# Kernel optimization log

Hardware: AMD Instinct MI355X
Metric: run time of the kernel (lower is better)

Reference implementation:

```python
import jax, jax.numpy as jnp
import numpy as np

N = 100000
IN_C = 128
HID = 32   # 2*out_channels
OUT = 16
NEG_SLOPE = 0.2


def gat_layer(x, src, dst, n, W, a_src, a_dst, b):
    # x: [n, Cin] -> h: [n, Cout]
    h = x @ W
    alpha_s = h @ a_src  # [n]
    alpha_d = h @ a_dst  # [n]
    e = jax.nn.leaky_relu(alpha_s[src] + alpha_d[dst], NEG_SLOPE)  # [E]
    # softmax over edges grouped by destination node (self-loops ensure no empty groups)
    m = jax.ops.segment_max(e, dst, num_segments=n)
    ex = jnp.exp(e - m[dst])
    s = jax.ops.segment_sum(ex, dst, num_segments=n)
    alpha = ex / s[dst]  # [E]
    out = jax.ops.segment_sum(h[src] * alpha[:, None], dst, num_segments=n)
    return out + b


def setup_inputs() -> dict:
    key = jax.random.key(0)
    ks = jax.random.split(key, 16)
    x = jax.random.normal(ks[0], (N, IN_C), dtype=jnp.float32)
    edge_index = jax.random.randint(ks[1], (2, 1600000), 0, N, dtype=jnp.int64)

    def glorot(k, shape):
        fan = shape[0] + (shape[1] if len(shape) > 1 else 1)
        return jax.random.normal(k, shape, dtype=jnp.float32) * jnp.sqrt(2.0 / fan)

    return {
        "x": x,
        "edge_index": edge_index,
        "W1": glorot(ks[2], (IN_C, HID)),
        "a1_src": glorot(ks[3], (HID,)),
        "a1_dst": glorot(ks[4], (HID,)),
        "b1": jnp.zeros((HID,), dtype=jnp.float32),
        "W_mu": glorot(ks[5], (HID, OUT)),
        "a_mu_src": glorot(ks[6], (OUT,)),
        "a_mu_dst": glorot(ks[7], (OUT,)),
        "b_mu": jnp.zeros((OUT,), dtype=jnp.float32),
        "W_ls": glorot(ks[8], (HID, OUT)),
        "a_ls_src": glorot(ks[9], (OUT,)),
        "a_ls_dst": glorot(ks[10], (OUT,)),
        "b_ls": jnp.zeros((OUT,), dtype=jnp.float32),
    }


def reference(x, edge_index, W1, a1_src, a1_dst, b1,
              W_mu, a_mu_src, a_mu_dst, b_mu,
              W_ls, a_ls_src, a_ls_dst, b_ls):
    n = x.shape[0]
    # PyG GATConv default: add self-loops
    loop = jnp.arange(n, dtype=edge_index.dtype)
    src = jnp.concatenate([edge_index[0], loop])
    dst = jnp.concatenate([edge_index[1], loop])

    h = jax.nn.relu(gat_layer(x, src, dst, n, W1, a1_src, a1_dst, b1))
    mu = gat_layer(h, src, dst, n, W_mu, a_mu_src, a_mu_dst, b_mu)
    logstd = gat_layer(h, src, dst, n, W_ls, a_ls_src, a_ls_dst, b_ls)
    return (mu, logstd)
```

## Files before the change

kernel.cpp:

```cpp
#include <hip/hip_runtime.h>
#include <hip/hip_bf16.h>
#include <hip/hip_fp16.h>

typedef unsigned int u32;
typedef unsigned short u16;

__device__ __forceinline__ float lrelu(float v) {
    return v > 0.f ? v : 0.2f * v;
}

__device__ __forceinline__ float4 ldq_h16(const u16* __restrict__ row, int q) {
    uint2 u = ((const uint2*)row)[q];
    __half2 a = *(__half2*)&u.x;
    __half2 b = *(__half2*)&u.y;
    float2 fa = __half22float2(a);
    float2 fb = __half22float2(b);
    return make_float4(fa.x, fa.y, fb.x, fb.y);
}

__device__ __forceinline__ u32 pack2h(float x, float y) {
    __half2 h = __float22half2_rn(make_float2(x, y));
    return *(u32*)&h;
}

#define PCHUNK 4096
#define NW 256

__global__ __launch_bounds__(256) void g1p_kernel(
    const float* __restrict__ x, const float* __restrict__ W,
    const float* __restrict__ a_src, const float* __restrict__ a_dst,
    u16* __restrict__ h16, float* __restrict__ as_, float* __restrict__ ad_,
    const int* __restrict__ srcI, const int* __restrict__ dstI,
    u32* __restrict__ pairs, u32* __restrict__ bcur,
    int n, int E, int wsz, int cap, int pgrid)
{
    __shared__ float xs[64][132];
    __shared__ float Wl[128][32];
    __shared__ float asv[32], adv[32];
    __shared__ u32 lcount[NW];
    __shared__ u32 lbase[NW];
    int t = threadIdx.x;

    if ((int)blockIdx.x < pgrid) {
        int chunk = blockIdx.x * PCHUNK;
        lcount[t] = 0;
        __syncthreads();
        u32 pk[16]; int wv[16]; u32 rk[16]; bool val[16];
#pragma unroll
        for (int k = 0; k < 16; k++) {
            int i = chunk + k * 256 + t;
            val[k] = i < E;
            if (val[k]) {
                u32 s = (u32)srcI[i];
                u32 d = (u32)dstI[i];
                wv[k] = d / (u32)wsz;
                u32 dloc = d - (u32)wv[k] * (u32)wsz;
                pk[k] = (dloc << 17) | s;
                rk[k] = atomicAdd(&lcount[wv[k]], 1u);
            }
        }
        __syncthreads();
        if (lcount[t] > 0)
            lbase[t] = atomicAdd(&bcur[t], lcount[t]);
        __syncthreads();
#pragma unroll
        for (int k = 0; k < 16; k++) {
            if (val[k]) {
                u32 pos = lbase[wv[k]] + rk[k];
                if (pos < (u32)cap)
                    pairs[(size_t)wv[k] * cap + pos] = pk[k];
            }
        }
        return;
    }

    int rb = (blockIdx.x - pgrid) * 64;

    for (int i = t; i < 4096; i += 256) Wl[i >> 5][i & 31] = W[i];
    if (t < 32) { asv[t] = a_src[t]; adv[t] = a_dst[t]; }
    for (int i = t; i < 2048; i += 256) {
        int row = i >> 5, seg = i & 31;
        float4 v = make_float4(0.f, 0.f, 0.f, 0.f);
        if (rb + row < n)
            v = ((const float4*)(x + (size_t)(rb + row) * 128))[seg];
        int c = seg * 4;
        xs[row][c + 0] = v.x; xs[row][c + 1] = v.y;
        xs[row][c + 2] = v.z; xs[row][c + 3] = v.w;
    }
    __syncthreads();

    int tr = t >> 3;
    int tc = t & 7;
    float acc[2][4];
#pragma unroll
    for (int i = 0; i < 2; i++)
#pragma unroll
        for (int j = 0; j < 4; j++) acc[i][j] = 0.f;

#pragma unroll 4
    for (int k = 0; k < 128; k++) {
        float x0 = xs[tr][k];
        float x1 = xs[tr + 32][k];
        float4 wv = *(const float4*)&Wl[k][tc * 4];
        acc[0][0] += x0 * wv.x; acc[0][1] += x0 * wv.y;
        acc[0][2] += x0 * wv.z; acc[0][3] += x0 * wv.w;
        acc[1][0] += x1 * wv.x; acc[1][1] += x1 * wv.y;
        acc[1][2] += x1 * wv.z; acc[1][3] += x1 * wv.w;
    }

#pragma unroll
    for (int i = 0; i < 2; i++) {
        int r = rb + tr + i * 32;
        if (r < n) {
            uint2 p;
            p.x = pack2h(acc[i][0], acc[i][1]);
            p.y = pack2h(acc[i][2], acc[i][3]);
            *(uint2*)&h16[(size_t)r * 32 + tc * 4] = p;
        }
        float ps = 0.f, pd = 0.f;
#pragma unroll
        for (int j = 0; j < 4; j++) {
            int c = tc * 4 + j;
            ps += acc[i][j] * asv[c];
            pd += acc[i][j] * adv[c];
        }
        for (int m = 1; m < 8; m <<= 1) {
            ps += __shfl_xor(ps, m, 64);
            pd += __shfl_xor(pd, m, 64);
        }
        if (tc == 0 && r < n) { as_[r] = ps; ad_[r] = pd; }
    }
}

__global__ __launch_bounds__(256) void csr_window_kernel(
    const u32* __restrict__ pairs, const u32* __restrict__ bcur,
    u32* __restrict__ rowS, u32* __restrict__ deg, int* __restrict__ srcS,
    int n, int wsz, int cap)
{
    __shared__ u32 dw[512];
    __shared__ u32 cw[512];
    __shared__ u32 ts[256];
    int grp = blockIdx.x;
    int t = threadIdx.x;
    int wlo = grp * wsz;
    int wnodes = n - wlo; if (wnodes < 0) wnodes = 0; if (wnodes > wsz) wnodes = wsz;
    u32 cnt = bcur[grp]; if (cnt > (u32)cap) cnt = (u32)cap;
    size_t base = (size_t)grp * cap;

    {
        int wlo_t = t * wsz;
        int wn_t = n - wlo_t; if (wn_t < 0) wn_t = 0; if (wn_t > wsz) wn_t = wsz;
        u32 c_t = bcur[t]; if (c_t > (u32)cap) c_t = (u32)cap;
        ts[t] = c_t + (u32)wn_t;
        __syncthreads();
        for (int o = 1; o < NW; o <<= 1) {
            u32 y = (t >= o) ? ts[t - o] : 0u;
            __syncthreads();
            ts[t] += y;
            __syncthreads();
        }
    }
    u32 wb = ts[grp] - (cnt + (u32)wnodes);
    __syncthreads();

    dw[t] = 0; dw[t + 256] = 0;
    __syncthreads();
    for (u32 i = t; i < cnt; i += 256)
        atomicAdd(&dw[pairs[base + i] >> 17], 1u);
    __syncthreads();

    int i0 = 2 * t, i1 = 2 * t + 1;
    u32 e0 = (i0 < wnodes) ? dw[i0] + 1u : 0u;
    u32 e1 = (i1 < wnodes) ? dw[i1] + 1u : 0u;
    ts[t] = e0 + e1;
    __syncthreads();
    for (int o = 1; o < 256; o <<= 1) {
        u32 y = (t >= o) ? ts[t - o] : 0u;
        __syncthreads();
        ts[t] += y;
        __syncthreads();
    }
    u32 off = wb + ts[t] - (e0 + e1);
    if (i0 < wnodes) {
        u32 dgi = dw[i0];
        cw[i0] = off;
        rowS[wlo + i0] = off;
        deg[wlo + i0] = dgi;
        srcS[off + dgi] = wlo + i0;
    }
    u32 off1 = off + e0;
    if (i1 < wnodes) {
        u32 dgi = dw[i1];
        cw[i1] = off1;
        rowS[wlo + i1] = off1;
        deg[wlo + i1] = dgi;
        srcS[off1 + dgi] = wlo + i1;
    }
    __syncthreads();

    for (u32 i = t; i < cnt; i += 256) {
        u32 pr = pairs[base + i];
        u32 pos = atomicAdd(&cw[pr >> 17], 1u);
        srcS[pos] = (int)(pr & 0x1FFFFu);
    }
}

__global__ __launch_bounds__(256) void l1_fused_kernel(
    const u32* __restrict__ rowS, const u32* __restrict__ deg,
    const int* __restrict__ srcS,
    const float* __restrict__ as_, const float* __restrict__ ad_,
    const u16* __restrict__ h16, const float* __restrict__ b1,
    float* __restrict__ h1r, int n)
{
    int d = blockIdx.x * 16 + (threadIdx.x >> 4);
    if (d >= n) return;
    int l  = threadIdx.x & 15;
    int e2 = l >> 3;
    int q  = l & 7;
    int gb = (threadIdx.x & 63) & 48;

    int beg = (int)rowS[d];
    int end = beg + (int)deg[d] + 1;
    float adv = ad_[d];

    float wsum = 0.f;
    float4 acc = make_float4(0.f, 0.f, 0.f, 0.f);

    for (int tb = beg; tb < end; tb += 16) {
        int j = tb + l;
        bool valid = j < end;
        int s = valid ? srcS[j] : 0;
        float p = valid ? __expf(fminf(lrelu(as_[s] + adv), 60.f)) : 0.f;
        int cnt = end - tb; if (cnt > 16) cnt = 16;
        for (int jj = 0; jj < cnt; jj += 2) {
            int idx = jj + e2;
            int sj  = __shfl(s, gb + idx, 64);
            float w = __shfl(p, gb + idx, 64);
            if (idx >= cnt) w = 0.f;
            wsum += w;
            float4 hv = ldq_h16(h16 + (size_t)sj * 32, q);
            acc.x += w * hv.x; acc.y += w * hv.y;
            acc.z += w * hv.z; acc.w += w * hv.w;
        }
    }
    wsum  += __shfl_xor(wsum, 8, 64);
    acc.x += __shfl_xor(acc.x, 8, 64);
    acc.y += __shfl_xor(acc.y, 8, 64);
    acc.z += __shfl_xor(acc.z, 8, 64);
    acc.w += __shfl_xor(acc.w, 8, 64);
    if (l < 8) {
        float inv = 1.f / wsum;
        float4 r;
        r.x = fmaxf(acc.x * inv + b1[4 * q + 0], 0.f);
        r.y = fmaxf(acc.y * inv + b1[4 * q + 1], 0.f);
        r.z = fmaxf(acc.z * inv + b1[4 * q + 2], 0.f);
        r.w = fmaxf(acc.w * inv + b1[4 * q + 3], 0.f);
        *(float4*)&h1r[(size_t)d * 32 + 4 * q] = r;
    }
}

__global__ __launch_bounds__(256) void gemm2_kernel(
    const float* __restrict__ h1r,
    const float* __restrict__ Wm, const float* __restrict__ Wl_,
    const float* __restrict__ ams, const float* __restrict__ amd,
    const float* __restrict__ alsb, const float* __restrict__ ald,
    u16* __restrict__ hmhl16, float2* __restrict__ attn2,
    float* __restrict__ amud, float* __restrict__ alsd, int n)
{
    __shared__ float hs[16][33];
    __shared__ float Wms[32][16], Wls[32][16];
    __shared__ float amsv[16], amdv[16], alsv[16], aldv[16];
    int t = threadIdx.x;
    int rb = blockIdx.x * 16;

    for (int i = t; i < 512; i += 256) {
        int k = i >> 4, c = i & 15;
        Wms[k][c] = Wm[i];
        Wls[k][c] = Wl_[i];
    }
    if (t < 16) {
        amsv[t] = ams[t]; amdv[t] = amd[t];
        alsv[t] = alsb[t]; aldv[t] = ald[t];
    }
    for (int i = t; i < 512; i += 256) {
        int r = i >> 5, k = i & 31;
        int gr = rb + r;
        hs[r][k] = (gr < n) ? h1r[(size_t)gr * 32 + k] : 0.f;
    }
    __syncthreads();

    int tr = t >> 4;
    int c = t & 15;
    float accm = 0.f, accl = 0.f;
#pragma unroll
    for (int k = 0; k < 32; k++) {
        float hv = hs[tr][k];
        accm += hv * Wms[k][c];
        accl += hv * Wls[k][c];
    }
    int r = rb + tr;
    if (r < n) {
        hmhl16[(size_t)r * 32 + c]      = __half_as_ushort(__float2half(accm));
        hmhl16[(size_t)r * 32 + 16 + c] = __half_as_ushort(__float2half(accl));
    }
    float pms = accm * amsv[c], pmd = accm * amdv[c];
    float pls = accl * alsv[c], pld = accl * aldv[c];
    for (int m = 1; m < 16; m <<= 1) {
        pms += __shfl_xor(pms, m, 64);
        pmd += __shfl_xor(pmd, m, 64);
        pls += __shfl_xor(pls, m, 64);
        pld += __shfl_xor(pld, m, 64);
    }
    if (c == 0 && r < n) {
        attn2[r] = make_float2(pms, pls);
        amud[r] = pmd;
        alsd[r] = pld;
    }
}

__global__ __launch_bounds__(256) void l2_fused_kernel(
    const u32* __restrict__ rowS, const u32* __restrict__ deg,
    const int* __restrict__ srcS,
    const float2* __restrict__ attn2,
    const float* __restrict__ amud, const float* __restrict__ alsd,
    const u16* __restrict__ hmhl16,
    const float* __restrict__ bm, const float* __restrict__ bl,
    float* __restrict__ out, int n)
{
    int d = blockIdx.x * 16 + (threadIdx.x >> 4);
    if (d >= n) return;
    int l  = threadIdx.x & 15;
    int e2 = l >> 3;
    int q  = l & 7;
    int gb = (threadIdx.x & 63) & 48;
    bool isMu = q < 4;

    int beg = (int)rowS[d];
    int end = beg + (int)deg[d] + 1;
    float amdv = amud[d], aldv = alsd[d];

    float wsum = 0.f;
    float4 acc = make_float4(0.f, 0.f, 0.f, 0.f);

    for (int tb = beg; tb < end; tb += 16) {
        int j = tb + l;
        bool valid = j < end;
        int s = valid ? srcS[j] : 0;
        float2 a2 = valid ? attn2[s] : make_float2(0.f, 0.f);
        float pm = valid ? __expf(fminf(lrelu(a2.x + amdv), 60.f)) : 0.f;
        float pl = valid ? __expf(fminf(lrelu(a2.y + aldv), 60.f)) : 0.f;
        int cnt = end - tb; if (cnt > 16) cnt = 16;
        for (int jj = 0; jj < cnt; jj += 2) {
            int idx = jj + e2;
            int sj    = __shfl(s, gb + idx, 64);
            float pmj = __shfl(pm, gb + idx, 64);
            float plj = __shfl(pl, gb + idx, 64);
            float w = isMu ? pmj : plj;
            if (idx >= cnt) w = 0.f;
            wsum += w;
            float4 hv = ldq_h16(hmhl16 + (size_t)sj * 32, q);
            acc.x += w * hv.x; acc.y += w * hv.y;
            acc.z += w * hv.z; acc.w += w * hv.w;
        }
    }
    wsum  += __shfl_xor(wsum, 8, 64);
    acc.x += __shfl_xor(acc.x, 8, 64);
    acc.y += __shfl_xor(acc.y, 8, 64);
    acc.z += __shfl_xor(acc.z, 8, 64);
    acc.w += __shfl_xor(acc.w, 8, 64);
    if (l < 8) {
        float inv = 1.f / wsum;
        if (q < 4) {
            float4 r;
            r.x = acc.x * inv + bm[4 * q + 0];
            r.y = acc.y * inv + bm[4 * q + 1];
            r.z = acc.z * inv + bm[4 * q + 2];
            r.w = acc.w * inv + bm[4 * q + 3];
            *(float4*)&out[(size_t)d * 16 + 4 * q] = r;
        } else {
            int qc = 4 * (q - 4);
            float4 r;
            r.x = acc.x * inv + bl[qc + 0];
            r.y = acc.y * inv + bl[qc + 1];
            r.z = acc.z * inv + bl[qc + 2];
            r.w = acc.w * inv + bl[qc + 3];
            *(float4*)&out[(size_t)n * 16 + (size_t)d * 16 + qc] = r;
        }
    }
}

extern "C" void kernel_launch(void* const* d_in, const int* in_sizes, int n_in,
                              void* d_out, int out_size, void* d_ws, size_t ws_size,
                              hipStream_t stream)
{
    const float* x   = (const float*)d_in[0];
    const int*   ei  = (const int*)d_in[1];
    const float* W1  = (const float*)d_in[2];
    const float* a1s = (const float*)d_in[3];
    const float* a1d = (const float*)d_in[4];
    const float* b1  = (const float*)d_in[5];
    const float* Wm  = (const float*)d_in[6];
    const float* ams = (const float*)d_in[7];
    const float* amd = (const float*)d_in[8];
    const float* bm  = (const float*)d_in[9];
    const float* Wl  = (const float*)d_in[10];
    const float* als = (const float*)d_in[11];
    const float* ald = (const float*)d_in[12];
    const float* bl  = (const float*)d_in[13];

    int n  = in_sizes[0] / 128;
    int E  = in_sizes[1] / 2;
    int Et = E + n;
    int wsz = (n + NW - 1) / NW;
    int cap = E / NW + 3072;
    const int* srcI = ei;
    const int* dstI = ei + E;

    float* ws = (float*)d_ws;
    u16*    h16   = (u16*)ws;
    u16*    hmhl16 = (u16*)(ws + (size_t)16 * n);
    float*  h1r  = ws + (size_t)32 * n;
    u32*    pairs = (u32*)(ws + (size_t)32 * n);
    float*  as_  = ws + (size_t)64 * n;
    float*  ad_  = ws + (size_t)65 * n;
    float2* attn2 = (float2*)(ws + (size_t)64 * n);
    float*  amud = ws + (size_t)66 * n;
    float*  alsd = ws + (size_t)67 * n;
    u32*    deg  = (u32*)(ws + (size_t)68 * n);
    u32*    bcur = (u32*)(ws + (size_t)69 * n);
    u32*    rowS = (u32*)(ws + (size_t)70 * n);
    int*    srcS = (int*)(ws + (size_t)71 * n);

    int pgrid = (E + PCHUNK - 1) / PCHUNK;
    int gblocks = (n + 63) / 64;

    hipMemsetAsync(bcur, 0, NW * sizeof(u32), stream);

    g1p_kernel<<<pgrid + gblocks, 256, 0, stream>>>(
        x, W1, a1s, a1d, h16, as_, ad_,
        srcI, dstI, pairs, bcur, n, E, wsz, cap, pgrid);

    csr_window_kernel<<<NW, 256, 0, stream>>>(pairs, bcur,
                                              rowS, deg, srcS, n, wsz, cap);

    l1_fused_kernel<<<(n + 15) / 16, 256, 0, stream>>>(rowS, deg, srcS, as_, ad_,
                                                       h16, b1, h1r, n);

    gemm2_kernel<<<(n + 15) / 16, 256, 0, stream>>>(h1r, Wm, Wl, ams, amd, als, ald,
                                                    hmhl16, attn2, amud, alsd, n);

    l2_fused_kernel<<<(n + 15) / 16, 256, 0, stream>>>(rowS, deg, srcS,
                                                       attn2, amud, alsd,
                                                       hmhl16, bm, bl,
                                                       (float*)d_out, n);
}
```

Measured before the change: 257.0 us.

## Sort destination nodes by degree within each window for balanced aggregation

The CSR build kernel now runs a per-window counting sort of destination nodes by in-degree and writes a permutation array. Both aggregation kernels read this permutation, so 16-lane groups in the same wavefront handle nodes with similar degree. The goal is less loop divergence and imbalance inside wavefronts. The cost is extra histogram and scan work in the CSR kernel, an extra indirection per node, and scattered writes to the output rows.

```diff
diff --git a/kernel.cpp b/kernel.cpp
--- a/kernel.cpp
+++ b/kernel.cpp
@@ -135,11 +135,13 @@
 __global__ __launch_bounds__(256) void csr_window_kernel(
     const u32* __restrict__ pairs, const u32* __restrict__ bcur,
     u32* __restrict__ rowS, u32* __restrict__ deg, int* __restrict__ srcS,
+    u32* __restrict__ perm,
     int n, int wsz, int cap)
 {
     __shared__ u32 dw[512];
     __shared__ u32 cw[512];
     __shared__ u32 ts[256];
+    __shared__ u32 hb[512];
     int grp = blockIdx.x;
     int t = threadIdx.x;
     int wlo = grp * wsz;
@@ -164,6 +166,7 @@
     __syncthreads();
 
     dw[t] = 0; dw[t + 256] = 0;
+    hb[t] = 0; hb[t + 256] = 0;
     __syncthreads();
     for (u32 i = t; i < cnt; i += 256)
         atomicAdd(&dw[pairs[base + i] >> 17], 1u);
@@ -198,6 +201,33 @@
     }
     __syncthreads();
 
+    for (int i = t; i < wnodes; i += 256)
+        atomicAdd(&hb[dw[i] < 511u ? dw[i] : 511u], 1u);
+    __syncthreads();
+    {
+        u32 h0 = hb[2 * t], h1 = hb[2 * t + 1];
+        ts[t] = h0 + h1;
+        __syncthreads();
+        for (int o = 1; o < 256; o <<= 1) {
+            u32 y = (t >= o) ? ts[t - o] : 0u;
+            __syncthreads();
+            ts[t] += y;
+            __syncthreads();
+        }
+        u32 b0 = ts[t] - (h0 + h1);
+        hb[2 * t] = b0;
+        hb[2 * t + 1] = b0 + h0;
+    }
+    __syncthreads();
+    for (int i = t; i < wnodes; i += 256) {
+        u32 dg = dw[i] < 511u ? dw[i] : 511u;
+        u32 pos = atomicAdd(&hb[dg], 1u);
+        perm[wlo + pos] = (u32)(wlo + i);
+    }
+    for (int i = wnodes + t; i < wsz; i += 256)
+        perm[wlo + i] = 0x7fffffffu;
+    __syncthreads();
+
     for (u32 i = t; i < cnt; i += 256) {
         u32 pr = pairs[base + i];
         u32 pos = atomicAdd(&cw[pr >> 17], 1u);
@@ -207,12 +237,14 @@
 
 __global__ __launch_bounds__(256) void l1_fused_kernel(
     const u32* __restrict__ rowS, const u32* __restrict__ deg,
-    const int* __restrict__ srcS,
+    const int* __restrict__ srcS, const u32* __restrict__ perm,
     const float* __restrict__ as_, const float* __restrict__ ad_,
     const u16* __restrict__ h16, const float* __restrict__ b1,
-    float* __restrict__ h1r, int n)
-{
-    int d = blockIdx.x * 16 + (threadIdx.x >> 4);
+    float* __restrict__ h1r, int n, int ntot)
+{
+    int gid = blockIdx.x * 16 + (threadIdx.x >> 4);
+    if (gid >= ntot) return;
+    int d = (int)perm[gid];
     if (d >= n) return;
     int l  = threadIdx.x & 15;
     int e2 = l >> 3;
@@ -320,14 +352,16 @@
 
 __global__ __launch_bounds__(256) void l2_fused_kernel(
     const u32* __restrict__ rowS, const u32* __restrict__ deg,
-    const int* __restrict__ srcS,
+    const int* __restrict__ srcS, const u32* __restrict__ perm,
     const float2* __restrict__ attn2,
     const float* __restrict__ amud, const float* __restrict__ alsd,
     const u16* __restrict__ hmhl16,
     const float* __restrict__ bm, const float* __restrict__ bl,
-    float* __restrict__ out, int n)
-{
-    int d = blockIdx.x * 16 + (threadIdx.x >> 4);
+    float* __restrict__ out, int n, int ntot)
+{
+    int gid = blockIdx.x * 16 + (threadIdx.x >> 4);
+    if (gid >= ntot) return;
+    int d = (int)perm[gid];
     if (d >= n) return;
     int l  = threadIdx.x & 15;
     int e2 = l >> 3;
@@ -413,6 +447,7 @@
     int Et = E + n;
     int wsz = (n + NW - 1) / NW;
     int cap = E / NW + 3072;
+    int ntot = NW * wsz;
     const int* srcI = ei;
     const int* dstI = ei + E;
 
@@ -430,6 +465,7 @@
     u32*    bcur = (u32*)(ws + (size_t)69 * n);
     u32*    rowS = (u32*)(ws + (size_t)70 * n);
     int*    srcS = (int*)(ws + (size_t)71 * n);
+    u32*    perm = (u32*)(ws + (size_t)71 * n + Et);
 
     int pgrid = (E + PCHUNK - 1) / PCHUNK;
     int gblocks = (n + 63) / 64;
@@ -441,16 +477,18 @@
         srcI, dstI, pairs, bcur, n, E, wsz, cap, pgrid);
 
     csr_window_kernel<<<NW, 256, 0, stream>>>(pairs, bcur,
-                                              rowS, deg, srcS, n, wsz, cap);
-
-    l1_fused_kernel<<<(n + 15) / 16, 256, 0, stream>>>(rowS, deg, srcS, as_, ad_,
-                                                       h16, b1, h1r, n);
+                                              rowS, deg, srcS, perm,
+                                              n, wsz, cap);
+
+    l1_fused_kernel<<<(ntot + 15) / 16, 256, 0, stream>>>(rowS, deg, srcS, perm,
+                                                          as_, ad_, h16, b1,
+                                                          h1r, n, ntot);
 
     gemm2_kernel<<<(n + 15) / 16, 256, 0, stream>>>(h1r, Wm, Wl, ams, amd, als, ald,
                                                     hmhl16, attn2, amud, alsd, n);
 
-    l2_fused_kernel<<<(n + 15) / 16, 256, 0, stream>>>(rowS, deg, srcS,
-                                                       attn2, amud, alsd,
-                                                       hmhl16, bm, bl,
-                                                       (float*)d_out, n);
-}
+    l2_fused_kernel<<<(ntot + 15) / 16, 256, 0, stream>>>(rowS, deg, srcS, perm,
+                                                          attn2, amud, alsd,
+                                                          hmhl16, bm, bl,
+                                                          (float*)d_out, n, ntot);
+}
```

New measurement: 254.7 us. No clear change (-0.9%).
